# Optimization experiments

Measured on AMD Instinct MI355X. Metric: run time of the kernel, lower is better.

The kernel has to match this reference:

```python
import jax, jax.numpy as jnp
import numpy as np

N = 4_000_000   # input points (nonzero voxels at tensor_stride 1)
B = 4           # batch size
G = 128         # voxel grid extent per axis at input stride
DIM = 3         # spatial dimension (init arg `dimension`)
STRIDE = 2      # kernel_size == stride == 2, dilation 1 -> coord // 2 pooling


def setup_inputs() -> dict:
    key = jax.random.key(0)
    k1, k2 = jax.random.split(key)
    batch_idx = jax.random.randint(k1, (N,), 0, B, dtype=jnp.int32)
    coords = jax.random.randint(k2, (N, DIM), 0, G, dtype=jnp.int32)
    # ME builds the "feature" tensor directly from the float coordinates
    coords_f = coords.astype(jnp.float32)
    return {"coords_f": coords_f, "batch_idx": batch_idx, "coords": coords,
            "grid_size": G}


def reference(coords_f, batch_idx, coords, grid_size):
    # Pooled (output) voxel per point: kernel==stride==2 => floor division.
    gs = grid_size // STRIDE                       # output grid extent per axis
    per_batch = gs ** DIM
    S = B * per_batch                              # dense output segment count

    out = coords // STRIDE                         # [N, 3] int
    lin = (out[:, 0] * gs + out[:, 1]) * gs + out[:, 2]
    seg = batch_idx * per_batch + lin              # [N] segment id in [0, S)

    ones = jnp.ones((coords_f.shape[0],), dtype=coords_f.dtype)
    # MinkowskiSumPooling on all-ones features = points per output voxel
    count = jax.ops.segment_sum(ones, seg, num_segments=S)          # [S]
    # MinkowskiGlobalSumPooling on ones = points per batch item
    glob = jax.ops.segment_sum(ones, batch_idx, num_segments=B)     # [B]

    seg_ids = jnp.arange(S)
    seg_batch = seg_ids // per_batch                                # [S]
    nonempty = count > 0
    # density = pool_xx / broadcast(pool_xx, glob_xx)
    density = jnp.where(nonempty, count / glob[seg_batch], 0.0)     # [S]

    # MinkowskiAvgPooling of coordinates -> per-voxel centroid
    csum = jax.ops.segment_sum(coords_f, seg, num_segments=S)       # [S, 3]
    safe_count = jnp.where(nonempty, count, 1.0)
    center = csum / safe_count[:, None]                             # [S, 3]

    # unpool(center) back to points, then sum-pool squared residuals
    mean_diff = coords_f - center[seg]                              # [N, 3]
    sqsum = jax.ops.segment_sum(mean_diff * mean_diff, seg, num_segments=S)
    variance = jnp.where(nonempty[:, None], sqsum / safe_count[:, None], 0.0)

    # Output-voxel coordinates (in original scale: multiples of STRIDE)
    rem = seg_ids % per_batch
    c0 = rem // (gs * gs)
    c1 = (rem // gs) % gs
    c2 = rem % gs
    out_coords = jnp.stack([c0, c1, c2], axis=-1).astype(coords_f.dtype) * STRIDE
    norm_center = jnp.where(nonempty[:, None], center - out_coords, 0.0)

    # ME.cat(density, variance, norm_center) -> [S, 2*DIM + 1]
    return jnp.concatenate([density[:, None], variance, norm_center], axis=1)
```

## Files before the change

kernel.cpp:

```cpp
#include <hip/hip_runtime.h>
#include <hip/hip_bf16.h>


#define BLOCK 256
#define PTS 2048
#define BUCKETS 256
#define SEG_SHIFT 12
#define SPB 4096
#define BLOCK2 1024

__device__ __forceinline__ unsigned make_pay(int b, int x, int y, int z, int gs) {
    const int seg = (((b * gs + (x >> 1)) * gs + (y >> 1)) * gs) + (z >> 1);
    return ((unsigned)seg << 3) | ((unsigned)(x & 1) << 2)
         | ((unsigned)(y & 1) << 1) | (unsigned)(z & 1);
}

__global__ __launch_bounds__(BLOCK)
void partition_kernel(const int* __restrict__ bidx,
                      const int* __restrict__ coords,
                      const int* __restrict__ gptr,
                      unsigned* __restrict__ payload,
                      unsigned* __restrict__ g_cursor,
                      int N, int CAP) {
    __shared__ unsigned s_pay[PTS];
    __shared__ unsigned s_hist[BUCKETS];
    __shared__ unsigned s_base[BUCKETS];
    __shared__ unsigned s_old[BUCKETS];
    __shared__ unsigned s_cur[BUCKETS];

    const int tid = threadIdx.x;
    s_hist[tid] = 0u;
    s_cur[tid] = 0u;
    __syncthreads();

    const int gs = gptr[0] >> 1;
    const int base = blockIdx.x * PTS;
    const int cnt = min(PTS, N - base);

    const int4* __restrict__ bidx4 = (const int4*)bidx;
    const int4* __restrict__ crd4  = (const int4*)coords;

    #pragma unroll
    for (int g = 0; g < PTS / (BLOCK * 4); ++g) {
        const int p0 = base + (g * BLOCK + tid) * 4;
        if (p0 + 3 < N) {
            const int q = p0 >> 2;
            const int4 b4 = bidx4[q];
            const int4 c0 = crd4[3 * q + 0];
            const int4 c1 = crd4[3 * q + 1];
            const int4 c2 = crd4[3 * q + 2];
            atomicAdd(&s_hist[make_pay(b4.x, c0.x, c0.y, c0.z, gs) >> (SEG_SHIFT + 3)], 1u);
            atomicAdd(&s_hist[make_pay(b4.y, c0.w, c1.x, c1.y, gs) >> (SEG_SHIFT + 3)], 1u);
            atomicAdd(&s_hist[make_pay(b4.z, c1.z, c1.w, c2.x, gs) >> (SEG_SHIFT + 3)], 1u);
            atomicAdd(&s_hist[make_pay(b4.w, c2.y, c2.z, c2.w, gs) >> (SEG_SHIFT + 3)], 1u);
        } else {
            for (int p = p0; p < N && p < p0 + 4; ++p) {
                const unsigned pay = make_pay(bidx[p], coords[3 * p + 0],
                                              coords[3 * p + 1], coords[3 * p + 2], gs);
                atomicAdd(&s_hist[pay >> (SEG_SHIFT + 3)], 1u);
            }
        }
    }
    __syncthreads();

    {
        const unsigned v = s_hist[tid];
        s_base[tid] = v;
        __syncthreads();
        for (int off = 1; off < BUCKETS; off <<= 1) {
            const unsigned t = (tid >= off) ? s_base[tid - off] : 0u;
            __syncthreads();
            s_base[tid] += t;
            __syncthreads();
        }
        const unsigned incl = s_base[tid];
        s_base[tid] = incl - v;
        s_old[tid] = atomicAdd(&g_cursor[tid], v);
        __syncthreads();
    }

    #pragma unroll
    for (int g = 0; g < PTS / (BLOCK * 4); ++g) {
        const int p0 = base + (g * BLOCK + tid) * 4;
        if (p0 + 3 < N) {
            const int q = p0 >> 2;
            const int4 b4 = bidx4[q];
            const int4 c0 = crd4[3 * q + 0];
            const int4 c1 = crd4[3 * q + 1];
            const int4 c2 = crd4[3 * q + 2];
            unsigned pay, bk, r;
            pay = make_pay(b4.x, c0.x, c0.y, c0.z, gs); bk = pay >> (SEG_SHIFT + 3);
            r = atomicAdd(&s_cur[bk], 1u); s_pay[s_base[bk] + r] = pay;
            pay = make_pay(b4.y, c0.w, c1.x, c1.y, gs); bk = pay >> (SEG_SHIFT + 3);
            r = atomicAdd(&s_cur[bk], 1u); s_pay[s_base[bk] + r] = pay;
            pay = make_pay(b4.z, c1.z, c1.w, c2.x, gs); bk = pay >> (SEG_SHIFT + 3);
            r = atomicAdd(&s_cur[bk], 1u); s_pay[s_base[bk] + r] = pay;
            pay = make_pay(b4.w, c2.y, c2.z, c2.w, gs); bk = pay >> (SEG_SHIFT + 3);
            r = atomicAdd(&s_cur[bk], 1u); s_pay[s_base[bk] + r] = pay;
        } else {
            for (int p = p0; p < N && p < p0 + 4; ++p) {
                const unsigned pay = make_pay(bidx[p], coords[3 * p + 0],
                                              coords[3 * p + 1], coords[3 * p + 2], gs);
                const unsigned bk = pay >> (SEG_SHIFT + 3);
                const unsigned r = atomicAdd(&s_cur[bk], 1u);
                s_pay[s_base[bk] + r] = pay;
            }
        }
    }
    __syncthreads();

    for (int j = tid; j < cnt; j += BLOCK) {
        const unsigned p = s_pay[j];
        const unsigned bk = p >> (SEG_SHIFT + 3);
        const unsigned off = s_old[bk] + ((unsigned)j - s_base[bk]);
        if (off < (unsigned)CAP)
            payload[(size_t)bk * CAP + off] = p;
    }
}

__global__ __launch_bounds__(BLOCK2)
void stats_kernel(const unsigned* __restrict__ payload,
                  const unsigned* __restrict__ g_cursor,
                  float* __restrict__ out, int CAP) {
    __shared__ unsigned fine[SPB];
    __shared__ unsigned s_g[64];

    const int tid = threadIdx.x;
    const int k = blockIdx.x;

    for (int s = tid; s < SPB; s += BLOCK2) fine[s] = 0u;
    if (tid < 64) s_g[tid] = g_cursor[(k & ~63) + tid];
    __syncthreads();
    for (int o = 32; o > 0; o >>= 1) {
        if (tid < o) s_g[tid] += s_g[tid + o];
        __syncthreads();
    }
    const float ginv = 1.0f / (float)s_g[0];

    unsigned cnt = g_cursor[k];
    if (cnt > (unsigned)CAP) cnt = (unsigned)CAP;
    const uint4* __restrict__ pay4 = (const uint4*)(payload + (size_t)k * CAP);
    const unsigned n4 = cnt >> 2;

    for (unsigned j = tid; j < n4; j += BLOCK2) {
        const uint4 p = pay4[j];
        atomicAdd(&fine[(p.x >> 3) & (SPB - 1)],
                  (1u << 24) | ((p.x & 4u) << 14) | ((p.x & 2u) << 7) | (p.x & 1u));
        atomicAdd(&fine[(p.y >> 3) & (SPB - 1)],
                  (1u << 24) | ((p.y & 4u) << 14) | ((p.y & 2u) << 7) | (p.y & 1u));
        atomicAdd(&fine[(p.z >> 3) & (SPB - 1)],
                  (1u << 24) | ((p.z & 4u) << 14) | ((p.z & 2u) << 7) | (p.z & 1u));
        atomicAdd(&fine[(p.w >> 3) & (SPB - 1)],
                  (1u << 24) | ((p.w & 4u) << 14) | ((p.w & 2u) << 7) | (p.w & 1u));
    }
    for (unsigned j = (n4 << 2) + tid; j < cnt; j += BLOCK2) {
        const unsigned p = payload[(size_t)k * CAP + j];
        atomicAdd(&fine[(p >> 3) & (SPB - 1)],
                  (1u << 24) | ((p & 4u) << 14) | ((p & 2u) << 7) | (p & 1u));
    }
    __syncthreads();

    for (int s = tid; s < SPB; s += BLOCK2) {
        const unsigned a = fine[s];
        const int c = (int)(a >> 24);
        float d0 = 0.f, vx = 0.f, vy = 0.f, vz = 0.f, mx = 0.f, my = 0.f, mz = 0.f;
        if (c > 0) {
            const float inv = 1.0f / (float)c;
            mx = (float)((a >> 16) & 0xffu) * inv;
            my = (float)((a >> 8) & 0xffu) * inv;
            mz = (float)(a & 0xffu) * inv;
            vx = mx - mx * mx;
            vy = my - my * my;
            vz = mz - mz * mz;
            d0 = (float)c * ginv;
        }
        float* row = out + (size_t)(k * SPB + s) * 7;
        row[0] = d0;
        row[1] = vx; row[2] = vy; row[3] = vz;
        row[4] = mx; row[5] = my; row[6] = mz;
    }
}

__global__ __launch_bounds__(BLOCK)
void accum_kernel(const int* __restrict__ bidx,
                  const int* __restrict__ coords,
                  const int* __restrict__ gptr,
                  unsigned* __restrict__ acc, int astride,
                  int* __restrict__ glob, int N) {
    __shared__ int gcnt[4];
    if (threadIdx.x < 4) gcnt[threadIdx.x] = 0;
    __syncthreads();
    const int gs = gptr[0] >> 1;
    int l0 = 0, l1 = 0, l2 = 0, l3 = 0;
    const int stride = gridDim.x * blockDim.x;
    for (int i = blockIdx.x * blockDim.x + threadIdx.x; i < N; i += stride) {
        const int b  = bidx[i];
        const int cx = coords[3 * i + 0];
        const int cy = coords[3 * i + 1];
        const int cz = coords[3 * i + 2];
        const int seg = (((b * gs + (cx >> 1)) * gs + (cy >> 1)) * gs) + (cz >> 1);
        const unsigned val = (1u << 24)
                           | ((unsigned)(cx & 1) << 16)
                           | ((unsigned)(cy & 1) << 8)
                           |  (unsigned)(cz & 1);
        atomicAdd(&acc[(size_t)seg * astride], val);
        l0 += (b == 0); l1 += (b == 1); l2 += (b == 2); l3 += (b == 3);
    }
    if (l0) atomicAdd(&gcnt[0], l0);
    if (l1) atomicAdd(&gcnt[1], l1);
    if (l2) atomicAdd(&gcnt[2], l2);
    if (l3) atomicAdd(&gcnt[3], l3);
    __syncthreads();
    if (threadIdx.x < 4 && gcnt[threadIdx.x] != 0)
        atomicAdd(&glob[threadIdx.x], gcnt[threadIdx.x]);
}

__global__ __launch_bounds__(BLOCK)
void finalize_kernel(const unsigned* __restrict__ acc, int astride,
                     const int* __restrict__ glob,
                     float* __restrict__ out, int S, int pbShift) {
    const int s = blockIdx.x * blockDim.x + threadIdx.x;
    if (s >= S) return;
    const unsigned a = acc[(size_t)s * astride];
    const int b = s >> pbShift;
    const int c = (int)(a >> 24);
    float d0 = 0.f, vx = 0.f, vy = 0.f, vz = 0.f, mx = 0.f, my = 0.f, mz = 0.f;
    if (c > 0) {
        const float inv = 1.0f / (float)c;
        mx = (float)((a >> 16) & 0xffu) * inv;
        my = (float)((a >> 8) & 0xffu) * inv;
        mz = (float)(a & 0xffu) * inv;
        vx = mx - mx * mx; vy = my - my * my; vz = mz - mz * mz;
        d0 = (float)c / (float)glob[b];
    }
    float* row = out + (size_t)s * 7;
    row[0] = d0;
    row[1] = vx; row[2] = vy; row[3] = vz;
    row[4] = mx; row[5] = my; row[6] = mz;
}

extern "C" void kernel_launch(void* const* d_in, const int* in_sizes, int n_in,
                              void* d_out, int out_size, void* d_ws, size_t ws_size,
                              hipStream_t stream) {
    const int* bidx   = (const int*)d_in[1];
    const int* coords = (const int*)d_in[2];
    const int* gptr   = (const int*)d_in[3];

    const int N = in_sizes[1];
    const int S = out_size / 7;
    const int per_batch = S / 4;

    const int NpB = (N + BUCKETS - 1) / BUCKETS;
    const int CAP = ((NpB + NpB / 8 + 64) + 63) & ~63;
    const size_t need = 1024 + (size_t)BUCKETS * (size_t)CAP * 4u;

    const bool fast = (S == (BUCKETS * SPB)) && (per_batch == (S / 4)) &&
                      (per_batch / SPB == 64) && (ws_size >= need) && (N > 0);

    if (fast) {
        unsigned* g_cursor = (unsigned*)d_ws;
        unsigned* payload  = (unsigned*)((char*)d_ws + 1024);
        hipMemsetAsync(d_ws, 0, 1024, stream);

        const int blocks = (N + PTS - 1) / PTS;
        partition_kernel<<<blocks, BLOCK, 0, stream>>>(
            bidx, coords, gptr, payload, g_cursor, N, CAP);
        stats_kernel<<<BUCKETS, BLOCK2, 0, stream>>>(
            payload, g_cursor, (float*)d_out, CAP);
    } else {
        int pbShift = 0;
        while ((1 << pbShift) < per_batch) ++pbShift;
        int* glob = (int*)d_ws;
        const size_t accBytes = (size_t)S * sizeof(unsigned);
        unsigned* acc;
        int astride;
        if (ws_size >= accBytes + 64) {
            acc = (unsigned*)((char*)d_ws + 64);
            astride = 1;
            hipMemsetAsync(d_ws, 0, 64 + accBytes, stream);
        } else {
            acc = (unsigned*)d_out;
            astride = 7;
            hipMemsetAsync(d_out, 0, (size_t)out_size * sizeof(float), stream);
            hipMemsetAsync(d_ws, 0, 64, stream);
        }
        int accBlocks = (N + BLOCK - 1) / BLOCK;
        if (accBlocks > 2048) accBlocks = 2048;
        accum_kernel<<<accBlocks, BLOCK, 0, stream>>>(bidx, coords, gptr,
                                                      acc, astride, glob, N);
        const int finBlocks = (S + BLOCK - 1) / BLOCK;
        finalize_kernel<<<finBlocks, BLOCK, 0, stream>>>(acc, astride, glob,
                                                         (float*)d_out, S, pbShift);
    }
}
```

Measured before the change: 173.5 us.

## Enlarge partition tiles and stage stats output through shared memory for coalesced stores

The partition kernel now uses 1024-thread blocks that each bin 8192 points, which cuts the number of blocks and the global cursor atomics per bucket, and lets each bucket write longer contiguous runs. The stats kernel now writes its 7-float rows into a shared-memory staging buffer and copies them out as float4 stores, replacing strided scalar writes to the 7-wide output. The change adds 28KB of shared memory and extra barriers to the stats kernel. It also raises shared-memory use per partition block, which may lower occupancy.

```diff
diff --git a/kernel.cpp b/kernel.cpp
--- a/kernel.cpp
+++ b/kernel.cpp
@@ -2,12 +2,13 @@
 #include <hip/hip_bf16.h>
 
 
-#define BLOCK 256
-#define PTS 2048
+#define BLOCK1 1024
+#define PTS 8192
 #define BUCKETS 256
 #define SEG_SHIFT 12
 #define SPB 4096
 #define BLOCK2 1024
+#define FBLOCK 256
 
 __device__ __forceinline__ unsigned make_pay(int b, int x, int y, int z, int gs) {
     const int seg = (((b * gs + (x >> 1)) * gs + (y >> 1)) * gs) + (z >> 1);
@@ -15,7 +16,7 @@
          | ((unsigned)(y & 1) << 1) | (unsigned)(z & 1);
 }
 
-__global__ __launch_bounds__(BLOCK)
+__global__ __launch_bounds__(BLOCK1, 8)
 void partition_kernel(const int* __restrict__ bidx,
                       const int* __restrict__ coords,
                       const int* __restrict__ gptr,
@@ -29,8 +30,7 @@
     __shared__ unsigned s_cur[BUCKETS];
 
     const int tid = threadIdx.x;
-    s_hist[tid] = 0u;
-    s_cur[tid] = 0u;
+    if (tid < BUCKETS) { s_hist[tid] = 0u; s_cur[tid] = 0u; }
     __syncthreads();
 
     const int gs = gptr[0] >> 1;
@@ -41,8 +41,8 @@
     const int4* __restrict__ crd4  = (const int4*)coords;
 
     #pragma unroll
-    for (int g = 0; g < PTS / (BLOCK * 4); ++g) {
-        const int p0 = base + (g * BLOCK + tid) * 4;
+    for (int g = 0; g < PTS / (BLOCK1 * 4); ++g) {
+        const int p0 = base + (g * BLOCK1 + tid) * 4;
         if (p0 + 3 < N) {
             const int q = p0 >> 2;
             const int4 b4 = bidx4[q];
@@ -64,24 +64,26 @@
     __syncthreads();
 
     {
-        const unsigned v = s_hist[tid];
-        s_base[tid] = v;
+        unsigned v = 0u;
+        if (tid < BUCKETS) { v = s_hist[tid]; s_base[tid] = v; }
         __syncthreads();
         for (int off = 1; off < BUCKETS; off <<= 1) {
-            const unsigned t = (tid >= off) ? s_base[tid - off] : 0u;
+            unsigned t = 0u;
+            if (tid < BUCKETS && tid >= off) t = s_base[tid - off];
             __syncthreads();
-            s_base[tid] += t;
+            if (tid < BUCKETS) s_base[tid] += t;
             __syncthreads();
         }
-        const unsigned incl = s_base[tid];
-        s_base[tid] = incl - v;
-        s_old[tid] = atomicAdd(&g_cursor[tid], v);
+        if (tid < BUCKETS) {
+            s_base[tid] -= v;
+            s_old[tid] = atomicAdd(&g_cursor[tid], v);
+        }
         __syncthreads();
     }
 
     #pragma unroll
-    for (int g = 0; g < PTS / (BLOCK * 4); ++g) {
-        const int p0 = base + (g * BLOCK + tid) * 4;
+    for (int g = 0; g < PTS / (BLOCK1 * 4); ++g) {
+        const int p0 = base + (g * BLOCK1 + tid) * 4;
         if (p0 + 3 < N) {
             const int q = p0 >> 2;
             const int4 b4 = bidx4[q];
@@ -109,7 +111,7 @@
     }
     __syncthreads();
 
-    for (int j = tid; j < cnt; j += BLOCK) {
+    for (int j = tid; j < cnt; j += BLOCK1) {
         const unsigned p = s_pay[j];
         const unsigned bk = p >> (SEG_SHIFT + 3);
         const unsigned off = s_old[bk] + ((unsigned)j - s_base[bk]);
@@ -123,6 +125,7 @@
                   const unsigned* __restrict__ g_cursor,
                   float* __restrict__ out, int CAP) {
     __shared__ unsigned fine[SPB];
+    __shared__ float s_stage[BLOCK2 * 7];
     __shared__ unsigned s_g[64];
 
     const int tid = threadIdx.x;
@@ -160,8 +163,8 @@
     }
     __syncthreads();
 
-    for (int s = tid; s < SPB; s += BLOCK2) {
-        const unsigned a = fine[s];
+    for (int t = 0; t < SPB; t += BLOCK2) {
+        const unsigned a = fine[t + tid];
         const int c = (int)(a >> 24);
         float d0 = 0.f, vx = 0.f, vy = 0.f, vz = 0.f, mx = 0.f, my = 0.f, mz = 0.f;
         if (c > 0) {
@@ -174,14 +177,24 @@
             vz = mz - mz * mz;
             d0 = (float)c * ginv;
         }
-        float* row = out + (size_t)(k * SPB + s) * 7;
-        row[0] = d0;
-        row[1] = vx; row[2] = vy; row[3] = vz;
-        row[4] = mx; row[5] = my; row[6] = mz;
-    }
-}
-
-__global__ __launch_bounds__(BLOCK)
+        float* st = &s_stage[tid * 7];
+        st[0] = d0;
+        st[1] = vx; st[2] = vy; st[3] = vz;
+        st[4] = mx; st[5] = my; st[6] = mz;
+        __syncthreads();
+
+        const float4* src = (const float4*)s_stage;
+        float4* dst = (float4*)(out + ((size_t)k * SPB + t) * 7);
+        #pragma unroll
+        for (int j = 0; j < (BLOCK2 * 7) / (4 * BLOCK2) + 1; ++j) {
+            const int idx = j * BLOCK2 + tid;
+            if (idx < (BLOCK2 * 7) / 4) dst[idx] = src[idx];
+        }
+        __syncthreads();
+    }
+}
+
+__global__ __launch_bounds__(FBLOCK)
 void accum_kernel(const int* __restrict__ bidx,
                   const int* __restrict__ coords,
                   const int* __restrict__ gptr,
@@ -215,7 +228,7 @@
         atomicAdd(&glob[threadIdx.x], gcnt[threadIdx.x]);
 }
 
-__global__ __launch_bounds__(BLOCK)
+__global__ __launch_bounds__(FBLOCK)
 void finalize_kernel(const unsigned* __restrict__ acc, int astride,
                      const int* __restrict__ glob,
                      float* __restrict__ out, int S, int pbShift) {
@@ -263,7 +276,7 @@
         hipMemsetAsync(d_ws, 0, 1024, stream);
 
         const int blocks = (N + PTS - 1) / PTS;
-        partition_kernel<<<blocks, BLOCK, 0, stream>>>(
+        partition_kernel<<<blocks, BLOCK1, 0, stream>>>(
             bidx, coords, gptr, payload, g_cursor, N, CAP);
         stats_kernel<<<BUCKETS, BLOCK2, 0, stream>>>(
             payload, g_cursor, (float*)d_out, CAP);
@@ -284,12 +297,12 @@
             hipMemsetAsync(d_out, 0, (size_t)out_size * sizeof(float), stream);
             hipMemsetAsync(d_ws, 0, 64, stream);
         }
-        int accBlocks = (N + BLOCK - 1) / BLOCK;
+        int accBlocks = (N + FBLOCK - 1) / FBLOCK;
         if (accBlocks > 2048) accBlocks = 2048;
-        accum_kernel<<<accBlocks, BLOCK, 0, stream>>>(bidx, coords, gptr,
-                                                      acc, astride, glob, N);
-        const int finBlocks = (S + BLOCK - 1) / BLOCK;
-        finalize_kernel<<<finBlocks, BLOCK, 0, stream>>>(acc, astride, glob,
-                                                         (float*)d_out, S, pbShift);
-    }
-}
+        accum_kernel<<<accBlocks, FBLOCK, 0, stream>>>(bidx, coords, gptr,
+                                                       acc, astride, glob, N);
+        const int finBlocks = (S + FBLOCK - 1) / FBLOCK;
+        finalize_kernel<<<finBlocks, FBLOCK, 0, stream>>>(acc, astride, glob,
+                                                          (float*)d_out, S, pbShift);
+    }
+}
```

Result: faster. 148.6 us (-14.4%).
